# Kernel optimization log

Hardware: AMD Instinct MI355X
Metric: run time of the kernel (lower is better)

Reference implementation:

```python
import jax, jax.numpy as jnp
import numpy as np

N_RAYS = 131072
N_PTS = 128
FAR = 1e10  # sentinel delta for the last sample, as in the torch code


def setup_inputs() -> dict:
    key = jax.random.key(0)
    k1, k2, k3 = jax.random.split(key, 3)
    # nonnegative densities (sigma)
    density = jax.random.uniform(k1, (N_RAYS, N_PTS), dtype=jnp.float32) * 2.0
    # per-sample RGB features
    feature = jax.random.uniform(k2, (N_RAYS, N_PTS, 3), dtype=jnp.float32)
    # monotonically increasing sample depths along each ray (near=0.1, far=6.1)
    depth_values = jnp.sort(
        jax.random.uniform(k3, (N_RAYS, N_PTS), dtype=jnp.float32) * 6.0 + 0.1,
        axis=-1,
    )
    return {"density": density, "feature": feature, "depth_values": depth_values}


def reference(density, feature, depth_values):
    # deltas: successive depth differences, huge value for the final sample  [N, P]
    deltas = jnp.concatenate(
        [depth_values[:, 1:] - depth_values[:, :-1],
         jnp.full_like(depth_values[:, :1], FAR)],
        axis=-1,
    )
    # per-sample transmittance factor t = exp(-sigma * delta)  [N, P]
    t = jnp.exp(-density * deltas)
    # exclusive cumulative transmittance T_i = prod_{j<i} t_j  (T_0 = 1)  [N, P]
    T = jnp.concatenate(
        [jnp.ones_like(t[:, :1]), jnp.cumprod(t, axis=1)[:, :-1]], axis=1
    )
    # alpha-compositing weights and RGB aggregation
    weights = T * (1.0 - t)                                  # [N, P]
    feat = jnp.sum(weights[..., None] * feature, axis=1)     # [N, 3]

    # depth estimate: torch code sets T>=1 entries to -inf, then selects T != -inf,
    # i.e. keeps samples where T < 1; normalizes t over selected samples.
    select = T < 1.0                                         # [N, P] bool
    t_sel = jnp.where(select, t, 0.0)
    denom = jnp.sum(t_sel, axis=1, keepdims=True)            # [N, 1]
    t_norm = t_sel / denom                                   # [N, P]
    depth = jnp.sum(t_norm * depth_values, axis=1)           # [N]
    depth = jnp.where(depth == 0.0, jnp.inf, depth)
    return feat, depth
```

## Files before the change

kernel.cpp:

```cpp
#include <hip/hip_runtime.h>
#include <math.h>

#define N_RAYS 131072
#define N_PTS  128
#define FAR_DELTA 1e10f

__global__ __launch_bounds__(256) void volrender_kernel(
    const float* __restrict__ density,
    const float* __restrict__ feature,
    const float* __restrict__ depthv,
    float* __restrict__ out)
{
    const int lane = threadIdx.x & 63;
    const int ray  = blockIdx.x * 4 + (threadIdx.x >> 6);
    if (ray >= N_RAYS) return;

    const size_t rbase = (size_t)ray * N_PTS + 2 * lane;
    const float2 dv = *reinterpret_cast<const float2*>(depthv  + rbase);
    const float2 sg = *reinterpret_cast<const float2*>(density + rbase);

    const float* fb = feature + (size_t)ray * N_PTS * 3 + 6 * lane;
    const float2 fA = *reinterpret_cast<const float2*>(fb);
    const float2 fB = *reinterpret_cast<const float2*>(fb + 2);
    const float2 fC = *reinterpret_cast<const float2*>(fb + 4);

    const float dnext  = __shfl_down(dv.x, 1);
    const float delta0 = dv.y - dv.x;
    const float delta1 = (lane == 63) ? FAR_DELTA : (dnext - dv.y);

    const float t0 = expf(-sg.x * delta0);
    const float t1 = expf(-sg.y * delta1);

    float scan = t0 * t1;
    #pragma unroll
    for (int off = 1; off < 64; off <<= 1) {
        const float v = __shfl_up(scan, off);
        if (lane >= off) scan *= v;
    }
    float excl = __shfl_up(scan, 1);
    if (lane == 0) excl = 1.0f;
    const float T0 = excl;
    const float T1 = excl * t0;

    const float w0 = T0 * (1.0f - t0);
    const float w1 = T1 * (1.0f - t1);
    float fx = w0 * fA.x + w1 * fB.y;
    float fy = w0 * fA.y + w1 * fC.x;
    float fz = w0 * fB.x + w1 * fC.y;

    const float ts0 = (T0 < 1.0f) ? t0 : 0.0f;
    const float ts1 = (T1 < 1.0f) ? t1 : 0.0f;
    float st = ts0 + ts1;
    float sd = ts0 * dv.x + ts1 * dv.y;

    #pragma unroll
    for (int off = 32; off > 0; off >>= 1) {
        fx += __shfl_xor(fx, off);
        fy += __shfl_xor(fy, off);
        fz += __shfl_xor(fz, off);
        st += __shfl_xor(st, off);
        sd += __shfl_xor(sd, off);
    }

    if (lane == 0) {
        out[(size_t)ray * 3 + 0] = fx;
        out[(size_t)ray * 3 + 1] = fy;
        out[(size_t)ray * 3 + 2] = fz;
        const float dep = sd / st;
        out[(size_t)N_RAYS * 3 + ray] = (dep == 0.0f) ? INFINITY : dep;
    }
}

extern "C" void kernel_launch(void* const* d_in, const int* in_sizes, int n_in,
                              void* d_out, int out_size, void* d_ws, size_t ws_size,
                              hipStream_t stream) {
    const float* density = (const float*)d_in[0];
    const float* feature = (const float*)d_in[1];
    const float* depthv  = (const float*)d_in[2];
    float* out = (float*)d_out;

    const int rays_per_block = 4;
    const int grid = N_RAYS / rays_per_block;
    volrender_kernel<<<grid, 256, 0, stream>>>(density, feature, depthv, out);
}
```

Measured before the change: 65.65 us.

## Map 16 lanes per ray with 8 samples each and DPP row scans

Each ray is now handled by 16 lanes, each owning 8 consecutive samples loaded with float4 vector loads. The thread-local prefix product is combined across lanes with a DPP row-shift scan, and the reductions use DPP row shifts instead of 64-wide shuffles. It also switches to __expf and sets a launch-bounds occupancy hint. The aim is to cut the cross-lane shuffle/LDS traffic and the scan depth, and to widen memory transactions. In exchange it uses more registers per thread and a less accurate exp.

```diff
diff --git a/kernel.cpp b/kernel.cpp
--- a/kernel.cpp
+++ b/kernel.cpp
@@ -5,64 +5,82 @@
 #define N_PTS  128
 #define FAR_DELTA 1e10f
 
-__global__ __launch_bounds__(256) void volrender_kernel(
+template<int CTRL>
+__device__ __forceinline__ float dpp_mov(float src, float old) {
+    return __builtin_bit_cast(float, __builtin_amdgcn_update_dpp(
+        __builtin_bit_cast(int, old), __builtin_bit_cast(int, src),
+        CTRL, 0xF, 0xF, false));
+}
+
+__global__ __launch_bounds__(256, 4) void volrender_kernel(
     const float* __restrict__ density,
     const float* __restrict__ feature,
     const float* __restrict__ depthv,
     float* __restrict__ out)
 {
-    const int lane = threadIdx.x & 63;
-    const int ray  = blockIdx.x * 4 + (threadIdx.x >> 6);
-    if (ray >= N_RAYS) return;
+    const int tid = threadIdx.x;
+    const int sub = tid & 15;
+    const int ray = blockIdx.x * 16 + (tid >> 4);
 
-    const size_t rbase = (size_t)ray * N_PTS + 2 * lane;
-    const float2 dv = *reinterpret_cast<const float2*>(depthv  + rbase);
-    const float2 sg = *reinterpret_cast<const float2*>(density + rbase);
+    const size_t sbase = (size_t)ray * N_PTS + sub * 8;
 
-    const float* fb = feature + (size_t)ray * N_PTS * 3 + 6 * lane;
-    const float2 fA = *reinterpret_cast<const float2*>(fb);
-    const float2 fB = *reinterpret_cast<const float2*>(fb + 2);
-    const float2 fC = *reinterpret_cast<const float2*>(fb + 4);
+    const float4 d0 = *reinterpret_cast<const float4*>(depthv + sbase);
+    const float4 d1 = *reinterpret_cast<const float4*>(depthv + sbase + 4);
+    const float4 g0 = *reinterpret_cast<const float4*>(density + sbase);
+    const float4 g1 = *reinterpret_cast<const float4*>(density + sbase + 4);
 
-    const float dnext  = __shfl_down(dv.x, 1);
-    const float delta0 = dv.y - dv.x;
-    const float delta1 = (lane == 63) ? FAR_DELTA : (dnext - dv.y);
+    const float* fb = feature + (size_t)ray * (N_PTS * 3) + sub * 24;
+    float ff[24];
+    #pragma unroll
+    for (int k = 0; k < 6; ++k)
+        *reinterpret_cast<float4*>(&ff[4 * k]) =
+            *reinterpret_cast<const float4*>(fb + 4 * k);
 
-    const float t0 = expf(-sg.x * delta0);
-    const float t1 = expf(-sg.y * delta1);
+    const float dv[8] = {d0.x, d0.y, d0.z, d0.w, d1.x, d1.y, d1.z, d1.w};
+    const float sg[8] = {g0.x, g0.y, g0.z, g0.w, g1.x, g1.y, g1.z, g1.w};
 
-    float scan = t0 * t1;
+    const float dn = dpp_mov<0x101>(d0.x, 0.0f);
+    float dl[8];
     #pragma unroll
-    for (int off = 1; off < 64; off <<= 1) {
-        const float v = __shfl_up(scan, off);
-        if (lane >= off) scan *= v;
-    }
-    float excl = __shfl_up(scan, 1);
-    if (lane == 0) excl = 1.0f;
-    const float T0 = excl;
-    const float T1 = excl * t0;
+    for (int j = 0; j < 7; ++j) dl[j] = dv[j + 1] - dv[j];
+    dl[7] = (sub == 15) ? FAR_DELTA : (dn - dv[7]);
 
-    const float w0 = T0 * (1.0f - t0);
-    const float w1 = T1 * (1.0f - t1);
-    float fx = w0 * fA.x + w1 * fB.y;
-    float fy = w0 * fA.y + w1 * fC.x;
-    float fz = w0 * fB.x + w1 * fC.y;
+    float t[8], p[8];
+    #pragma unroll
+    for (int j = 0; j < 8; ++j) t[j] = __expf(-sg[j] * dl[j]);
+    p[0] = t[0];
+    #pragma unroll
+    for (int j = 1; j < 8; ++j) p[j] = p[j - 1] * t[j];
 
-    const float ts0 = (T0 < 1.0f) ? t0 : 0.0f;
-    const float ts1 = (T1 < 1.0f) ? t1 : 0.0f;
-    float st = ts0 + ts1;
-    float sd = ts0 * dv.x + ts1 * dv.y;
+    float scan = p[7];
+    scan *= dpp_mov<0x111>(scan, 1.0f);
+    scan *= dpp_mov<0x112>(scan, 1.0f);
+    scan *= dpp_mov<0x114>(scan, 1.0f);
+    scan *= dpp_mov<0x118>(scan, 1.0f);
+    const float excl = dpp_mov<0x111>(scan, 1.0f);
 
+    float fx = 0.f, fy = 0.f, fz = 0.f, st = 0.f, sd = 0.f;
     #pragma unroll
-    for (int off = 32; off > 0; off >>= 1) {
-        fx += __shfl_xor(fx, off);
-        fy += __shfl_xor(fy, off);
-        fz += __shfl_xor(fz, off);
-        st += __shfl_xor(st, off);
-        sd += __shfl_xor(sd, off);
+    for (int j = 0; j < 8; ++j) {
+        const float T = (j == 0) ? excl : excl * p[j - 1];
+        const float w = fmaf(-T, t[j], T);
+        fx = fmaf(w, ff[3 * j + 0], fx);
+        fy = fmaf(w, ff[3 * j + 1], fy);
+        fz = fmaf(w, ff[3 * j + 2], fz);
+        const float ts = (T < 1.0f) ? t[j] : 0.0f;
+        st += ts;
+        sd = fmaf(ts, dv[j], sd);
     }
 
-    if (lane == 0) {
+    #define RED16(x)                 \
+        x += dpp_mov<0x108>(x, 0.f); \
+        x += dpp_mov<0x104>(x, 0.f); \
+        x += dpp_mov<0x102>(x, 0.f); \
+        x += dpp_mov<0x101>(x, 0.f);
+    RED16(fx) RED16(fy) RED16(fz) RED16(st) RED16(sd)
+    #undef RED16
+
+    if (sub == 0) {
         out[(size_t)ray * 3 + 0] = fx;
         out[(size_t)ray * 3 + 1] = fy;
         out[(size_t)ray * 3 + 2] = fz;
@@ -79,7 +97,6 @@
     const float* depthv  = (const float*)d_in[2];
     float* out = (float*)d_out;
 
-    const int rays_per_block = 4;
-    const int grid = N_RAYS / rays_per_block;
+    const int grid = N_RAYS / 16;
     volrender_kernel<<<grid, 256, 0, stream>>>(density, feature, depthv, out);
 }
```

Result: no change. 66.68 us (+1.6%).
